# Kernel tuning notes

Measured on AMD Instinct MI355X. Metric: run time of the kernel, lower is better.

Reference implementation:

```python
import jax, jax.numpy as jnp
import numpy as np

H, D = 16, 64            # heads_num, mouse_hidden_dim // heads_num
START_FRAME = 9728       # current_start (token units)
GLOBAL_END_PREV = 9728   # kv_cache['global_end_index'] before this call
LOCAL_END_PREV = 9728    # kv_cache['local_end_index'] before this call
SINK = 0                 # sink_tokens in source
WINDOW = 8192            # max_attention_size = local_attn_size (token units)


def _rope_interleaved(x, cos_h, sin_h):
    # non-neox (interleaved) rotary: x [B,S,H,D], cos_h/sin_h [S, D//2]
    x1 = x[..., 0::2]
    x2 = x[..., 1::2]
    c = cos_h[None, :, None, :]
    s = sin_h[None, :, None, :]
    o1 = x1 * c - x2 * s
    o2 = x2 * c + x1 * s
    return jnp.stack([o1, o2], axis=-1).reshape(x.shape)


def setup_inputs() -> dict:
    key = jax.random.key(0)
    ks = jax.random.split(key, 7)
    B, S, C = 1, 1024, 10240
    return {
        'q': jax.random.normal(ks[0], (B, S, H, D), jnp.float32),
        'k': jax.random.normal(ks[1], (B, S, H, D), jnp.float32),
        'v': jax.random.normal(ks[2], (B, S, H, D), jnp.float32),
        'cache_k': jax.random.normal(ks[3], (B, C, H, D), jnp.float32),
        'cache_v': jax.random.normal(ks[4], (B, C, H, D), jnp.float32),
        'freqs_cos': jax.random.uniform(ks[5], (START_FRAME + S, D), jnp.float32, -1.0, 1.0),
        'freqs_sin': jax.random.uniform(ks[6], (START_FRAME + S, D), jnp.float32, -1.0, 1.0),
    }


def reference(q, k, v, cache_k, cache_v, freqs_cos, freqs_sin):
    B, S, _, _ = q.shape
    # _apply_rotary_emb_qk: slice freqs at start_offset, take every-other col (cos_half)
    cos_h = freqs_cos[START_FRAME:START_FRAME + S, ::2]  # [S, D//2]
    sin_h = freqs_sin[START_FRAME:START_FRAME + S, ::2]
    q_r = _rope_interleaved(q, cos_h, sin_h)
    k_r = _rope_interleaved(k, cos_h, sin_h)

    # ring-buffer KV-cache update (all index math is static Python ints)
    current_end = START_FRAME + S
    cache_size = cache_k.shape[1]
    num_new = S
    if current_end > GLOBAL_END_PREV and num_new + LOCAL_END_PREV > cache_size:
        num_evicted = num_new + LOCAL_END_PREV - cache_size
        num_rolled = LOCAL_END_PREV - num_evicted - SINK
        rolled_k = jax.lax.dynamic_slice_in_dim(cache_k, SINK + num_evicted, num_rolled, axis=1)
        rolled_v = jax.lax.dynamic_slice_in_dim(cache_v, SINK + num_evicted, num_rolled, axis=1)
        cache_k = cache_k.at[:, SINK:SINK + num_rolled].set(rolled_k)
        cache_v = cache_v.at[:, SINK:SINK + num_rolled].set(rolled_v)
        local_end = LOCAL_END_PREV + current_end - GLOBAL_END_PREV - num_evicted
    else:
        local_end = LOCAL_END_PREV + current_end - GLOBAL_END_PREV
    local_start = local_end - num_new
    cache_k = cache_k.at[:, local_start:local_end].set(k_r)
    cache_v = cache_v.at[:, local_start:local_end].set(v)

    # windowed (last local_attn_size tokens) non-causal attention
    cache_start = max(0, local_end - WINDOW)
    wk = cache_k[:, cache_start:local_end]  # [B, W, H, D]
    wv = cache_v[:, cache_start:local_end]
    scale = 1.0 / np.float32(np.sqrt(D))
    scores = jnp.einsum('bqhd,bkhd->bhqk', q_r, wk) * scale
    probs = jax.nn.softmax(scores, axis=-1)
    out = jnp.einsum('bhqk,bkhd->bqhd', probs, wv)
    return out.reshape(B, S, H * D)
```

## Files before the change

### kernel.cpp

```cpp
#include <hip/hip_runtime.h>

#define HH 16
#define DD 64
#define SQ 1024
#define LW 8192
#define OLDK 7168
#define CACHE_BASE 2560
#define SFRAME 9728
#define KSPLIT 4
#define KPER (LW / KSPLIT)
#define NSTEP (KPER / 64)

#define KB_OFF 0u
#define VT_OFF 16777216u
#define QB_OFF 33554432u
#define OP_OFF 35651584u
#define LP_OFF 52428800u

typedef __bf16 bf16x8 __attribute__((ext_vector_type(8)));
typedef float floatx16 __attribute__((ext_vector_type(16)));

__device__ __forceinline__ unsigned short f2bf(float f) {
  unsigned u = __builtin_bit_cast(unsigned, f);
  u += 0x7fffu + ((u >> 16) & 1u);
  return (unsigned short)(u >> 16);
}

__device__ __forceinline__ float fast_exp2(float x) {
#if __has_builtin(__builtin_amdgcn_exp2f)
  return __builtin_amdgcn_exp2f(x);
#else
  return __builtin_exp2f(x);
#endif
}

__device__ __forceinline__ void async16(void* lds, const void* g) {
  __builtin_amdgcn_global_load_lds((__attribute__((address_space(1))) void*)(g),
                                   (__attribute__((address_space(3))) void*)(lds),
                                   16, 0, 0);
}

__global__ __launch_bounds__(256) void prepass(
    const float* __restrict__ qin, const float* __restrict__ kin,
    const float* __restrict__ vin, const float* __restrict__ ck,
    const float* __restrict__ cv, const float* __restrict__ fc,
    const float* __restrict__ fs, unsigned short* __restrict__ Kb,
    unsigned short* __restrict__ Vt, unsigned short* __restrict__ Qb) {
  int b = blockIdx.x, t = threadIdx.x;
  if (b < 2048) {
    __shared__ float tl[64 * 65];
    int h = b >> 7, kk0 = (b & 127) * 64;
    int col = t & 63, rb = t >> 6;
#pragma unroll
    for (int i = 0; i < 16; i++) {
      int r = i * 4 + rb;
      int kk = kk0 + r;
      float val = (kk < OLDK) ? cv[(CACHE_BASE + kk) * (HH * DD) + h * DD + col]
                              : vin[(kk - OLDK) * (HH * DD) + h * DD + col];
      tl[r * 65 + col] = val;
    }
    __syncthreads();
#pragma unroll
    for (int i = 0; i < 16; i++) {
      int d = i * 4 + rb;
      Vt[(h * DD + d) * LW + kk0 + col] = f2bf(tl[col * 65 + d]);
    }
  } else if (b < 9216) {
    int b1 = b - 2048;
    int h = b1 / 448, g = b1 % 448;
    int kk = g * 16 + (t >> 4);
    int lane = t & 15;
    float4 val = *(const float4*)(ck + (CACHE_BASE + kk) * (HH * DD) + h * DD + lane * 4);
    ushort4 o;
    o.x = f2bf(val.x); o.y = f2bf(val.y); o.z = f2bf(val.z); o.w = f2bf(val.w);
    *(ushort4*)(Kb + (h * LW + kk) * DD + lane * 4) = o;
  } else if (b < 11264) {
    int b2 = b - 9216;
    int rh = b2 * 8 + (t >> 5);
    int s = rh >> 4, h = rh & 15, i = t & 31;
    float2 x = *(const float2*)(kin + s * (HH * DD) + h * DD + 2 * i);
    float c = fc[(SFRAME + s) * DD + 2 * i];
    float sn = fs[(SFRAME + s) * DD + 2 * i];
    ushort2 o;
    o.x = f2bf(x.x * c - x.y * sn);
    o.y = f2bf(x.y * c + x.x * sn);
    *(ushort2*)(Kb + (h * LW + OLDK + s) * DD + 2 * i) = o;
  } else {
    int b3 = b - 11264;
    int rh = b3 * 8 + (t >> 5);
    int s = rh >> 4, h = rh & 15, i = t & 31;
    const float SC = 0.18033688011112042f;
    float2 x = *(const float2*)(qin + s * (HH * DD) + h * DD + 2 * i);
    float c = fc[(SFRAME + s) * DD + 2 * i];
    float sn = fs[(SFRAME + s) * DD + 2 * i];
    ushort2 o;
    o.x = f2bf((x.x * c - x.y * sn) * SC);
    o.y = f2bf((x.y * c + x.x * sn) * SC);
    *(ushort2*)(Qb + (h * SQ + s) * DD + 2 * i) = o;
  }
}

__global__ __launch_bounds__(256) void attn(
    const unsigned short* __restrict__ Kb, const unsigned short* __restrict__ Vt,
    const unsigned short* __restrict__ Qb, float* __restrict__ Op,
    float* __restrict__ Lp) {
  __shared__ __align__(16) unsigned char sK[8192];
  __shared__ __align__(16) unsigned char sV[8192];
  __shared__ __align__(16) unsigned char sP[4 * 32 * 144];

  int bid = blockIdx.x;
  int g = bid & 63, qb = bid >> 6;
  int h = g & 15, ks = g >> 4;
  int t = threadIdx.x;
  int w = t >> 6, lane = t & 63;
  int l31 = lane & 31, e = lane >> 5;
  int sw = l31 & 7;
  int qrow = qb * 128 + w * 32 + l31;

  bf16x8 qf[4];
  const unsigned short* qptr = Qb + (h * SQ + qrow) * DD + 8 * e;
#pragma unroll
  for (int c = 0; c < 4; c++) qf[c] = *(const bf16x8*)(qptr + 16 * c);

  floatx16 oA, oB;
#pragma unroll
  for (int i = 0; i < 16; i++) { oA[i] = 0.f; oB[i] = 0.f; }
  float lsum = 0.f;

  const unsigned short* KbH = Kb + h * (LW * DD);
  const unsigned short* VtH = Vt + h * (DD * LW);
  int kkBase = ks * KPER;
  unsigned char* prow = sP + (w * 32 + l31) * 144;

  for (int st = 0; st < NSTEP; st++) {
    int kk0 = kkBase + st * 64;
    __syncthreads();
#pragma unroll
    for (int hf = 0; hf < 2; hf++) {
      int gi = w * 128 + hf * 64 + lane;
      int rr = gi >> 3;
      int bs = (gi & 7) ^ (rr & 7);
      async16(sK + gi * 16, KbH + (kk0 + rr) * DD + bs * 8);
      async16(sV + gi * 16, VtH + rr * LW + kk0 + bs * 8);
    }
    __syncthreads();

    floatx16 stA, stB;
#pragma unroll
    for (int i = 0; i < 16; i++) { stA[i] = 0.f; stB[i] = 0.f; }
#pragma unroll
    for (int c = 0; c < 4; c++) {
      int gsl = (2 * c + e) ^ sw;
      bf16x8 ka = *(const bf16x8*)(sK + (l31 * 8 + gsl) * 16);
      bf16x8 kb = *(const bf16x8*)(sK + ((l31 + 32) * 8 + gsl) * 16);
      stA = __builtin_amdgcn_mfma_f32_32x32x16_bf16(ka, qf[c], stA, 0, 0, 0);
      stB = __builtin_amdgcn_mfma_f32_32x32x16_bf16(kb, qf[c], stB, 0, 0, 0);
    }

    float ps = 0.f;
#pragma unroll
    for (int i = 0; i < 16; i++) { stA[i] = fast_exp2(stA[i]); ps += stA[i]; }
#pragma unroll
    for (int i = 0; i < 16; i++) { stB[i] = fast_exp2(stB[i]); ps += stB[i]; }
    lsum += ps;

#pragma unroll
    for (int mt = 0; mt < 2; mt++) {
#pragma unroll
      for (int t4 = 0; t4 < 4; t4++) {
        float v0 = mt ? stB[4 * t4 + 0] : stA[4 * t4 + 0];
        float v1 = mt ? stB[4 * t4 + 1] : stA[4 * t4 + 1];
        float v2 = mt ? stB[4 * t4 + 2] : stA[4 * t4 + 2];
        float v3 = mt ? stB[4 * t4 + 3] : stA[4 * t4 + 3];
        unsigned u0 = __builtin_bit_cast(unsigned, v0) + 0x8000u;
        unsigned u1 = __builtin_bit_cast(unsigned, v1) + 0x8000u;
        unsigned u2 = __builtin_bit_cast(unsigned, v2) + 0x8000u;
        unsigned u3 = __builtin_bit_cast(unsigned, v3) + 0x8000u;
        uint2 pk;
        pk.x = __builtin_amdgcn_perm(u1, u0, 0x07060302);
        pk.y = __builtin_amdgcn_perm(u3, u2, 0x07060302);
        *(uint2*)(prow + 64 * mt + 16 * t4 + 8 * e) = pk;
      }
    }

#pragma unroll
    for (int kc = 0; kc < 4; kc++) {
      int gsl = (2 * kc + e) ^ sw;
      bf16x8 va = *(const bf16x8*)(sV + (l31 * 8 + gsl) * 16);
      bf16x8 vb = *(const bf16x8*)(sV + ((l31 + 32) * 8 + gsl) * 16);
      bf16x8 pf = *(const bf16x8*)(prow + 32 * kc + 16 * e);
      oA = __builtin_amdgcn_mfma_f32_32x32x16_bf16(va, pf, oA, 0, 0, 0);
      oB = __builtin_amdgcn_mfma_f32_32x32x16_bf16(vb, pf, oB, 0, 0, 0);
    }
  }

  lsum += __shfl_xor(lsum, 32, 64);
  float* op = Op + (((ks * 16 + h) * SQ) + qrow) * DD;
#pragma unroll
  for (int t4 = 0; t4 < 4; t4++) {
    float4 a, b;
    a.x = oA[4 * t4 + 0]; a.y = oA[4 * t4 + 1]; a.z = oA[4 * t4 + 2]; a.w = oA[4 * t4 + 3];
    b.x = oB[4 * t4 + 0]; b.y = oB[4 * t4 + 1]; b.z = oB[4 * t4 + 2]; b.w = oB[4 * t4 + 3];
    *(float4*)(op + 8 * t4 + 4 * e) = a;
    *(float4*)(op + 32 + 8 * t4 + 4 * e) = b;
  }
  if (e == 0) Lp[(ks * 16 + h) * SQ + qrow] = lsum;
}

__global__ __launch_bounds__(256) void combine(const float* __restrict__ Op,
                                               const float* __restrict__ Lp,
                                               float* __restrict__ out) {
  int idx = blockIdx.x * 256 + threadIdx.x;
  int d = idx & 63, q = (idx >> 6) & 1023, h = idx >> 16;
  float num = 0.f, den = 0.f;
#pragma unroll
  for (int s = 0; s < KSPLIT; s++) {
    int row = (s * 16 + h) * SQ + q;
    num += Op[row * DD + d];
    den += Lp[row];
  }
  out[q * (HH * DD) + h * DD + d] = num / den;
}

extern "C" void kernel_launch(void* const* d_in, const int* in_sizes, int n_in,
                              void* d_out, int out_size, void* d_ws, size_t ws_size,
                              hipStream_t stream) {
  const float* q  = (const float*)d_in[0];
  const float* k  = (const float*)d_in[1];
  const float* v  = (const float*)d_in[2];
  const float* ck = (const float*)d_in[3];
  const float* cv = (const float*)d_in[4];
  const float* fc = (const float*)d_in[5];
  const float* fs = (const float*)d_in[6];
  float* out = (float*)d_out;
  char* ws = (char*)d_ws;

  unsigned short* Kb = (unsigned short*)(ws + KB_OFF);
  unsigned short* Vt = (unsigned short*)(ws + VT_OFF);
  unsigned short* Qb = (unsigned short*)(ws + QB_OFF);
  float* Op = (float*)(ws + OP_OFF);
  float* Lp = (float*)(ws + LP_OFF);

  prepass<<<13312, 256, 0, stream>>>(q, k, v, ck, cv, fc, fs, Kb, Vt, Qb);
  attn<<<512, 256, 0, stream>>>(Kb, Vt, Qb, Op, Lp);
  combine<<<4096, 256, 0, stream>>>(Op, Lp, out);
}
```

Baseline: 186.6 us.

## Double per-wave query tile, keep P in registers via permlane swap, split keys 8-way

Each wave now processes 64 query rows instead of 32, so each K/V tile loaded into LDS feeds twice as many MFMAs. The probability matrix is no longer written to and reread from LDS; it is packed to bf16 with a hardware convert and rearranged across lanes with permlane32_swap. The key dimension is split 8 ways instead of 4 to keep the block count at 512, and launch bounds request 2 blocks per CU. The cost is higher register pressure from four accumulator tiles, and the combine step reads twice as many partial results.

```diff
diff --git a/kernel.cpp b/kernel.cpp
--- a/kernel.cpp
+++ b/kernel.cpp
@@ -7,7 +7,7 @@
 #define OLDK 7168
 #define CACHE_BASE 2560
 #define SFRAME 9728
-#define KSPLIT 4
+#define KSPLIT 8
 #define KPER (LW / KSPLIT)
 #define NSTEP (KPER / 64)
 
@@ -15,10 +15,12 @@
 #define VT_OFF 16777216u
 #define QB_OFF 33554432u
 #define OP_OFF 35651584u
-#define LP_OFF 52428800u
+#define LP_OFF 69206016u
 
 typedef __bf16 bf16x8 __attribute__((ext_vector_type(8)));
 typedef float floatx16 __attribute__((ext_vector_type(16)));
+typedef unsigned uintx2 __attribute__((ext_vector_type(2)));
+typedef unsigned uintx4 __attribute__((ext_vector_type(4)));
 
 __device__ __forceinline__ unsigned short f2bf(float f) {
   unsigned u = __builtin_bit_cast(unsigned, f);
@@ -31,6 +33,18 @@
   return __builtin_amdgcn_exp2f(x);
 #else
   return __builtin_exp2f(x);
+#endif
+}
+
+__device__ __forceinline__ unsigned pack_bf2(float a, float b) {
+#if __has_builtin(__builtin_amdgcn_cvt_pk_bf16_f32)
+  typedef __bf16 bf16x2_t __attribute__((ext_vector_type(2)));
+  bf16x2_t r = __builtin_amdgcn_cvt_pk_bf16_f32(a, b);
+  return __builtin_bit_cast(unsigned, r);
+#else
+  unsigned ua = __builtin_bit_cast(unsigned, a) + 0x8000u;
+  unsigned ub = __builtin_bit_cast(unsigned, b) + 0x8000u;
+  return __builtin_amdgcn_perm(ub, ua, 0x07060302);
 #endif
 }
 
@@ -100,37 +114,42 @@
   }
 }
 
-__global__ __launch_bounds__(256) void attn(
+__global__ __launch_bounds__(256, 2) void attn(
     const unsigned short* __restrict__ Kb, const unsigned short* __restrict__ Vt,
     const unsigned short* __restrict__ Qb, float* __restrict__ Op,
     float* __restrict__ Lp) {
   __shared__ __align__(16) unsigned char sK[8192];
   __shared__ __align__(16) unsigned char sV[8192];
-  __shared__ __align__(16) unsigned char sP[4 * 32 * 144];
 
   int bid = blockIdx.x;
-  int g = bid & 63, qb = bid >> 6;
+  int g = bid & 127, qb = bid >> 7;
   int h = g & 15, ks = g >> 4;
   int t = threadIdx.x;
   int w = t >> 6, lane = t & 63;
   int l31 = lane & 31, e = lane >> 5;
   int sw = l31 & 7;
-  int qrow = qb * 128 + w * 32 + l31;
-
-  bf16x8 qf[4];
-  const unsigned short* qptr = Qb + (h * SQ + qrow) * DD + 8 * e;
-#pragma unroll
-  for (int c = 0; c < 4; c++) qf[c] = *(const bf16x8*)(qptr + 16 * c);
-
-  floatx16 oA, oB;
-#pragma unroll
-  for (int i = 0; i < 16; i++) { oA[i] = 0.f; oB[i] = 0.f; }
-  float lsum = 0.f;
+  int q0 = qb * 256 + w * 64;
+
+  bf16x8 qf[2][4];
+#pragma unroll
+  for (int tq = 0; tq < 2; tq++) {
+    const unsigned short* qptr = Qb + (h * SQ + q0 + 32 * tq + l31) * DD + 8 * e;
+#pragma unroll
+    for (int c = 0; c < 4; c++) qf[tq][c] = *(const bf16x8*)(qptr + 16 * c);
+  }
+
+  floatx16 o[2][2];
+#pragma unroll
+  for (int a = 0; a < 2; a++)
+#pragma unroll
+    for (int bb = 0; bb < 2; bb++)
+#pragma unroll
+      for (int i = 0; i < 16; i++) o[a][bb][i] = 0.f;
+  float ls[2] = {0.f, 0.f};
 
   const unsigned short* KbH = Kb + h * (LW * DD);
   const unsigned short* VtH = Vt + h * (DD * LW);
   int kkBase = ks * KPER;
-  unsigned char* prow = sP + (w * 32 + l31) * 144;
 
   for (int st = 0; st < NSTEP; st++) {
     int kk0 = kkBase + st * 64;
@@ -145,41 +164,58 @@
     }
     __syncthreads();
 
-    floatx16 stA, stB;
-#pragma unroll
-    for (int i = 0; i < 16; i++) { stA[i] = 0.f; stB[i] = 0.f; }
+    floatx16 s[2][2];
+#pragma unroll
+    for (int a = 0; a < 2; a++)
+#pragma unroll
+      for (int bb = 0; bb < 2; bb++)
+#pragma unroll
+        for (int i = 0; i < 16; i++) s[a][bb][i] = 0.f;
 #pragma unroll
     for (int c = 0; c < 4; c++) {
       int gsl = (2 * c + e) ^ sw;
       bf16x8 ka = *(const bf16x8*)(sK + (l31 * 8 + gsl) * 16);
       bf16x8 kb = *(const bf16x8*)(sK + ((l31 + 32) * 8 + gsl) * 16);
-      stA = __builtin_amdgcn_mfma_f32_32x32x16_bf16(ka, qf[c], stA, 0, 0, 0);
-      stB = __builtin_amdgcn_mfma_f32_32x32x16_bf16(kb, qf[c], stB, 0, 0, 0);
-    }
-
-    float ps = 0.f;
-#pragma unroll
-    for (int i = 0; i < 16; i++) { stA[i] = fast_exp2(stA[i]); ps += stA[i]; }
-#pragma unroll
-    for (int i = 0; i < 16; i++) { stB[i] = fast_exp2(stB[i]); ps += stB[i]; }
-    lsum += ps;
-
-#pragma unroll
-    for (int mt = 0; mt < 2; mt++) {
-#pragma unroll
-      for (int t4 = 0; t4 < 4; t4++) {
-        float v0 = mt ? stB[4 * t4 + 0] : stA[4 * t4 + 0];
-        float v1 = mt ? stB[4 * t4 + 1] : stA[4 * t4 + 1];
-        float v2 = mt ? stB[4 * t4 + 2] : stA[4 * t4 + 2];
-        float v3 = mt ? stB[4 * t4 + 3] : stA[4 * t4 + 3];
-        unsigned u0 = __builtin_bit_cast(unsigned, v0) + 0x8000u;
-        unsigned u1 = __builtin_bit_cast(unsigned, v1) + 0x8000u;
-        unsigned u2 = __builtin_bit_cast(unsigned, v2) + 0x8000u;
-        unsigned u3 = __builtin_bit_cast(unsigned, v3) + 0x8000u;
-        uint2 pk;
-        pk.x = __builtin_amdgcn_perm(u1, u0, 0x07060302);
-        pk.y = __builtin_amdgcn_perm(u3, u2, 0x07060302);
-        *(uint2*)(prow + 64 * mt + 16 * t4 + 8 * e) = pk;
+      s[0][0] = __builtin_amdgcn_mfma_f32_32x32x16_bf16(ka, qf[0][c], s[0][0], 0, 0, 0);
+      s[0][1] = __builtin_amdgcn_mfma_f32_32x32x16_bf16(kb, qf[0][c], s[0][1], 0, 0, 0);
+      s[1][0] = __builtin_amdgcn_mfma_f32_32x32x16_bf16(ka, qf[1][c], s[1][0], 0, 0, 0);
+      s[1][1] = __builtin_amdgcn_mfma_f32_32x32x16_bf16(kb, qf[1][c], s[1][1], 0, 0, 0);
+    }
+
+    unsigned pk[2][2][4][2];
+#pragma unroll
+    for (int tq = 0; tq < 2; tq++) {
+#pragma unroll
+      for (int tk = 0; tk < 2; tk++) {
+#pragma unroll
+        for (int i = 0; i < 16; i++) s[tq][tk][i] = fast_exp2(s[tq][tk][i]);
+        float ps = 0.f;
+#pragma unroll
+        for (int i = 0; i < 16; i++) ps += s[tq][tk][i];
+        ls[tq] += ps;
+#pragma unroll
+        for (int b = 0; b < 4; b++)
+#pragma unroll
+          for (int p = 0; p < 2; p++)
+            pk[tq][tk][b][p] = pack_bf2(s[tq][tk][4 * b + 2 * p], s[tq][tk][4 * b + 2 * p + 1]);
+      }
+    }
+
+    bf16x8 pf[2][4];
+#pragma unroll
+    for (int tq = 0; tq < 2; tq++) {
+#pragma unroll
+      for (int tk = 0; tk < 2; tk++) {
+#pragma unroll
+        for (int kcp = 0; kcp < 2; kcp++) {
+          uintx2 r0 = __builtin_amdgcn_permlane32_swap(pk[tq][tk][2 * kcp][0],
+                                                       pk[tq][tk][2 * kcp + 1][0], false, false);
+          uintx2 r1 = __builtin_amdgcn_permlane32_swap(pk[tq][tk][2 * kcp][1],
+                                                       pk[tq][tk][2 * kcp + 1][1], false, false);
+          uintx4 f;
+          f[0] = r0[0]; f[1] = r1[0]; f[2] = r0[1]; f[3] = r1[1];
+          pf[tq][2 * tk + kcp] = __builtin_bit_cast(bf16x8, f);
+        }
       }
     }
 
@@ -188,23 +224,31 @@
       int gsl = (2 * kc + e) ^ sw;
       bf16x8 va = *(const bf16x8*)(sV + (l31 * 8 + gsl) * 16);
       bf16x8 vb = *(const bf16x8*)(sV + ((l31 + 32) * 8 + gsl) * 16);
-      bf16x8 pf = *(const bf16x8*)(prow + 32 * kc + 16 * e);
-      oA = __builtin_amdgcn_mfma_f32_32x32x16_bf16(va, pf, oA, 0, 0, 0);
-      oB = __builtin_amdgcn_mfma_f32_32x32x16_bf16(vb, pf, oB, 0, 0, 0);
-    }
-  }
-
-  lsum += __shfl_xor(lsum, 32, 64);
-  float* op = Op + (((ks * 16 + h) * SQ) + qrow) * DD;
-#pragma unroll
-  for (int t4 = 0; t4 < 4; t4++) {
-    float4 a, b;
-    a.x = oA[4 * t4 + 0]; a.y = oA[4 * t4 + 1]; a.z = oA[4 * t4 + 2]; a.w = oA[4 * t4 + 3];
-    b.x = oB[4 * t4 + 0]; b.y = oB[4 * t4 + 1]; b.z = oB[4 * t4 + 2]; b.w = oB[4 * t4 + 3];
-    *(float4*)(op + 8 * t4 + 4 * e) = a;
-    *(float4*)(op + 32 + 8 * t4 + 4 * e) = b;
-  }
-  if (e == 0) Lp[(ks * 16 + h) * SQ + qrow] = lsum;
+      o[0][0] = __builtin_amdgcn_mfma_f32_32x32x16_bf16(va, pf[0][kc], o[0][0], 0, 0, 0);
+      o[0][1] = __builtin_amdgcn_mfma_f32_32x32x16_bf16(vb, pf[0][kc], o[0][1], 0, 0, 0);
+      o[1][0] = __builtin_amdgcn_mfma_f32_32x32x16_bf16(va, pf[1][kc], o[1][0], 0, 0, 0);
+      o[1][1] = __builtin_amdgcn_mfma_f32_32x32x16_bf16(vb, pf[1][kc], o[1][1], 0, 0, 0);
+    }
+  }
+
+#pragma unroll
+  for (int tq = 0; tq < 2; tq++) {
+    float l = ls[tq];
+    l += __shfl_xor(l, 32, 64);
+    int qrow = q0 + 32 * tq + l31;
+    float* op = Op + (((ks * 16 + h) * SQ) + qrow) * DD;
+#pragma unroll
+    for (int t4 = 0; t4 < 4; t4++) {
+      float4 a, b;
+      a.x = o[tq][0][4 * t4 + 0]; a.y = o[tq][0][4 * t4 + 1];
+      a.z = o[tq][0][4 * t4 + 2]; a.w = o[tq][0][4 * t4 + 3];
+      b.x = o[tq][1][4 * t4 + 0]; b.y = o[tq][1][4 * t4 + 1];
+      b.z = o[tq][1][4 * t4 + 2]; b.w = o[tq][1][4 * t4 + 3];
+      *(float4*)(op + 8 * t4 + 4 * e) = a;
+      *(float4*)(op + 32 + 8 * t4 + 4 * e) = b;
+    }
+    if (e == 0) Lp[(ks * 16 + h) * SQ + qrow] = l;
+  }
 }
 
 __global__ __launch_bounds__(256) void combine(const float* __restrict__ Op,
```

Result: no change. 186.6 us (+0.0%).
